# Optimization experiments

Measured on AMD Instinct MI355X. Metric: run time of the kernel, lower is better.

Reference implementation:

```python
import jax, jax.numpy as jnp
import numpy as np

B, T, D = 2, 2048, 1024
H, DH = 16, 64  # heads, head_dim; inner_dim = H*DH = D
EPS = 1e-6


def _rmsnorm(x, g):
    # torch.nn.RMSNorm over last dim with affine weight g
    return x * jax.lax.rsqrt(jnp.mean(x * x, axis=-1, keepdims=True) + EPS) * g


def _interleaved_rope(x, cos, sin):
    # x: [B, T, D]; pairs (x0, x1) rotated: rot = [-x1, x0, -x3, x2, ...]
    b, t, d = x.shape
    x2 = x.reshape(b, t, d // 2, 2)
    rot = jnp.stack([-x2[..., 1], x2[..., 0]], axis=-1).reshape(b, t, d)
    return x * cos + rot * sin


def setup_inputs() -> dict:
    key = jax.random.key(0)
    ks = jax.random.split(key, 8)
    hidden_states = jax.random.normal(ks[0], (B, T, D), dtype=jnp.float32)
    cos = jax.random.uniform(ks[1], (1, T, D), dtype=jnp.float32)
    sin = jax.random.uniform(ks[2], (1, T, D), dtype=jnp.float32)
    s = 0.02  # init scale for weights
    wq = jax.random.normal(ks[3], (D, D), dtype=jnp.float32) * s
    wk = jax.random.normal(ks[4], (D, D), dtype=jnp.float32) * s
    wv = jax.random.normal(ks[5], (D, D), dtype=jnp.float32) * s
    wo = jax.random.normal(ks[6], (D, D), dtype=jnp.float32) * s
    bq = jnp.zeros((D,), jnp.float32)
    bk = jnp.zeros((D,), jnp.float32)
    bv = jnp.zeros((D,), jnp.float32)
    bo = jnp.zeros((D,), jnp.float32)
    gq = jnp.ones((D,), jnp.float32)
    gk = jnp.ones((D,), jnp.float32)
    return {
        'hidden_states': hidden_states, 'cos': cos, 'sin': sin,
        'wq': wq, 'bq': bq, 'wk': wk, 'bk': bk, 'wv': wv, 'bv': bv,
        'gq': gq, 'gk': gk, 'wo': wo, 'bo': bo,
    }


def reference(hidden_states, cos, sin, wq, bq, wk, bk, wv, bv, gq, gk, wo, bo):
    # QKV projections (weights stored as [in, out]) + RMSNorm(q,k) + RoPE
    q = _interleaved_rope(_rmsnorm(hidden_states @ wq + bq, gq), cos, sin)
    k = _interleaved_rope(_rmsnorm(hidden_states @ wk + bk, gk), cos, sin)
    v = hidden_states @ wv + bv

    # split heads: [B, T, D] -> [B, H, T, DH]
    def split(x):
        return x.reshape(B, T, H, DH).transpose(0, 2, 1, 3)
    q, k, v = split(q), split(k), split(v)

    scale = 1.0 / jnp.sqrt(jnp.float32(DH))
    scores = jnp.einsum('bhqd,bhkd->bhqk', q, k) * scale
    attn = jax.nn.softmax(scores, axis=-1)
    out = jnp.einsum('bhqk,bhkd->bhqd', attn, v)

    # merge heads + output projection
    out = out.transpose(0, 2, 1, 3).reshape(B, T, D)
    return out @ wo + bo
```

## Files before the change

kernel.cpp:

```cpp
#include <hip/hip_runtime.h>

typedef _Float16 f16;
typedef _Float16 f16x8 __attribute__((ext_vector_type(8)));
typedef _Float16 f16x4 __attribute__((ext_vector_type(4)));
typedef _Float16 f16x2 __attribute__((ext_vector_type(2)));
typedef float f32x4 __attribute__((ext_vector_type(4)));

#define MFMA(a, b, c) __builtin_amdgcn_mfma_f32_16x16x32_f16(a, b, c, 0, 0, 0)
#define PKRTZ(a, b) __builtin_bit_cast(f16x2, __builtin_amdgcn_cvt_pkrtz(a, b))

__device__ __forceinline__ void gload16(const void* g, void* l) {
  __builtin_amdgcn_global_load_lds((const __attribute__((address_space(1))) char*)g,
                                   (__attribute__((address_space(3))) char*)l, 16, 0, 0);
}


__global__ __launch_bounds__(256) void k_cvt_hidden(const float* __restrict__ x, f16* __restrict__ y) {
  int i = blockIdx.x * 256 + threadIdx.x;
  float4 v = ((const float4*)x)[i];
  f16x4 h; h[0] = (f16)v.x; h[1] = (f16)v.y; h[2] = (f16)v.z; h[3] = (f16)v.w;
  ((f16x4*)y)[i] = h;
}

__global__ __launch_bounds__(256) void k_cvt_w(const float* __restrict__ w0, const float* __restrict__ w1,
                                               const float* __restrict__ w2, const float* __restrict__ w3,
                                               f16* __restrict__ wt) {
  int z = blockIdx.z;
  const float* w = z == 0 ? w0 : z == 1 ? w1 : z == 2 ? w2 : w3;
  f16* dst = wt + (size_t)z * 1024 * 1024;
  __shared__ float tile[64][65];
  int t = threadIdx.x;
  int k0 = blockIdx.x * 64, n0 = blockIdx.y * 64;
  int cr = t >> 4, cc = (t & 15) * 4;
#pragma unroll
  for (int p = 0; p < 4; p++) {
    int r = cr + p * 16;
    float4 v = *(const float4*)&w[(size_t)(k0 + r) * 1024 + n0 + cc];
    tile[r][cc + 0] = v.x; tile[r][cc + 1] = v.y; tile[r][cc + 2] = v.z; tile[r][cc + 3] = v.w;
  }
  __syncthreads();
#pragma unroll
  for (int p = 0; p < 4; p++) {
    int nn = cr + p * 16;
    f16x4 h;
    h[0] = (f16)tile[cc + 0][nn]; h[1] = (f16)tile[cc + 1][nn];
    h[2] = (f16)tile[cc + 2][nn]; h[3] = (f16)tile[cc + 3][nn];
    *(f16x4*)&dst[(size_t)(n0 + nn) * 1024 + k0 + cc] = h;
  }
}

template <bool OUTF32>
__device__ __forceinline__ void gemm_core(const f16* __restrict__ A, const f16* __restrict__ Wrows,
                                          const float* __restrict__ bias, int m0,
                                          f16* __restrict__ oh, float* __restrict__ of) {
  __shared__ f16 Al[2][128 * 64];
  __shared__ f16 Bl[2][128 * 64];
  const int t = threadIdx.x;
  const int lane = t & 63, wid = t >> 6;
  const int lr = lane & 15, lg = lane >> 4;
  const int wm = wid >> 1, wn = wid & 1;
  const int lrow = lane >> 3;
  const int cb = (((lane & 7) ^ lrow) << 4);

  f32x4 acc[4][4] = {};

  auto stage = [&](int k0, int bs) {
#pragma unroll
    for (int it = 0; it < 4; it++) {
      int rbase = it * 32 + wid * 8;
      int row = rbase + lrow;
      gload16((const char*)&A[(size_t)(m0 + row) * 1024 + k0] + cb, (char*)&Al[bs][0] + rbase * 128);
      gload16((const char*)&Wrows[(size_t)row * 1024 + k0] + cb, (char*)&Bl[bs][0] + rbase * 128);
    }
  };

  stage(0, 0);
  __syncthreads();
  int cur = 0;
  for (int k0 = 0; k0 < 1024; k0 += 64) {
    if (k0 + 64 < 1024) stage(k0 + 64, cur ^ 1);
    f16x8 af[2][4], bf[2][4];
#pragma unroll
    for (int x = 0; x < 4; x++) {
      int ra = wm * 64 + x * 16 + lr;
      int rb = wn * 64 + x * 16 + lr;
#pragma unroll
      for (int kh = 0; kh < 2; kh++) {
        int ca = (kh * 64 + lg * 16) ^ ((lr & 7) << 4);
        af[kh][x] = *(const f16x8*)((char*)&Al[cur][0] + ra * 128 + ca);
        bf[kh][x] = *(const f16x8*)((char*)&Bl[cur][0] + rb * 128 + ca);
      }
    }
    __builtin_amdgcn_s_setprio(1);
#pragma unroll
    for (int kh = 0; kh < 2; kh++)
#pragma unroll
      for (int mt = 0; mt < 4; mt++)
#pragma unroll
        for (int nt = 0; nt < 4; nt++)
          acc[mt][nt] = MFMA(af[kh][mt], bf[kh][nt], acc[mt][nt]);
    __builtin_amdgcn_s_setprio(0);
    __syncthreads();
    cur ^= 1;
  }
#pragma unroll
  for (int mt = 0; mt < 4; mt++) {
#pragma unroll
    for (int nt = 0; nt < 4; nt++) {
      int col = wn * 64 + nt * 16 + lr;
      float bcol = bias[col];
#pragma unroll
      for (int e = 0; e < 4; e++) {
        int row = m0 + wm * 64 + mt * 16 + lg * 4 + e;
        float val = acc[mt][nt][e] + bcol;
        if (OUTF32) of[(size_t)row * 1024 + col] = val;
        else        oh[(size_t)row * 1024 + col] = (f16)val;
      }
    }
  }
}

__global__ __launch_bounds__(256, 2) void k_gemm_qkv(const f16* __restrict__ A, const f16* __restrict__ wt,
                                                     const float* __restrict__ bq, const float* __restrict__ bk,
                                                     const float* __restrict__ bv,
                                                     f16* __restrict__ q, f16* __restrict__ k, f16* __restrict__ v) {
  int n0 = blockIdx.y * 128;
  int zsel = n0 >> 10, cbs = n0 & 1023;
  const float* bias = (zsel == 0 ? bq : zsel == 1 ? bk : bv) + cbs;
  f16* dst = (zsel == 0 ? q : zsel == 1 ? k : v) + cbs;
  gemm_core<false>(A, wt + (size_t)n0 * 1024, bias, blockIdx.x * 128, dst, nullptr);
}

__global__ __launch_bounds__(256, 2) void k_gemm_o(const f16* __restrict__ A, const f16* __restrict__ wt3,
                                                   const float* __restrict__ bo, float* __restrict__ out) {
  int n0 = blockIdx.y * 128;
  gemm_core<true>(A, wt3 + (size_t)n0 * 1024, bo + n0, blockIdx.x * 128, nullptr, out + n0);
}

__global__ __launch_bounds__(256) void k_normrope(f16* __restrict__ qh, f16* __restrict__ kh,
                                                  const float* __restrict__ gq, const float* __restrict__ gk,
                                                  const float* __restrict__ cs, const float* __restrict__ sn) {
  int row = blockIdx.x, which = blockIdx.y;
  f16* buf = which ? kh : qh;
  const float* g = which ? gk : gq;
  int t = threadIdx.x, c4 = t * 4;
  f16x4 xv = *(const f16x4*)&buf[(size_t)row * 1024 + c4];
  float x0 = xv[0], x1 = xv[1], x2 = xv[2], x3 = xv[3];
  float ss = x0 * x0 + x1 * x1 + x2 * x2 + x3 * x3;
#pragma unroll
  for (int off = 1; off < 64; off <<= 1) ss += __shfl_xor(ss, off);
  __shared__ float red[4];
  if ((t & 63) == 0) red[t >> 6] = ss;
  __syncthreads();
  float inv = rsqrtf((red[0] + red[1] + red[2] + red[3]) * (1.0f / 1024.0f) + 1e-6f);
  int tt = row & 2047;
  float4 cv = *(const float4*)&cs[(size_t)tt * 1024 + c4];
  float4 sv = *(const float4*)&sn[(size_t)tt * 1024 + c4];
  float4 gv = *(const float4*)&g[c4];
  float y0 = x0 * inv * gv.x, y1 = x1 * inv * gv.y, y2 = x2 * inv * gv.z, y3 = x3 * inv * gv.w;
  f16x4 ov;
  ov[0] = (f16)(y0 * cv.x - y1 * sv.x);
  ov[1] = (f16)(y1 * cv.y + y0 * sv.y);
  ov[2] = (f16)(y2 * cv.z - y3 * sv.z);
  ov[3] = (f16)(y3 * cv.w + y2 * sv.w);
  *(f16x4*)&buf[(size_t)row * 1024 + c4] = ov;
}

__global__ __launch_bounds__(256) void k_vtrans(const f16* __restrict__ vh, f16* __restrict__ vt) {
  __shared__ f16 tile[64][65];
  int t = threadIdx.x;
  int t0 = blockIdx.x * 64;
  int bh = blockIdx.y;
  int b = bh >> 4, h = bh & 15;
  int rr = t >> 3, c8 = (t & 7) * 8;
#pragma unroll
  for (int p = 0; p < 2; p++) {
    int r = p * 32 + rr;
    f16x8 v = *(const f16x8*)&vh[(size_t)(b * 2048 + t0 + r) * 1024 + h * 64 + c8];
#pragma unroll
    for (int j = 0; j < 8; j++) tile[r][c8 + j] = v[j];
  }
  __syncthreads();
#pragma unroll
  for (int p = 0; p < 2; p++) {
    int dh = p * 32 + rr;
    f16x8 o;
#pragma unroll
    for (int j = 0; j < 8; j++) o[j] = tile[c8 + j][dh];
    *(f16x8*)&vt[((size_t)bh * 64 + dh) * 2048 + t0 + c8] = o;
  }
}

#define ASWZ(row) ((((row) & 3) | (((row) & 8) >> 1)) << 4)

__global__ __launch_bounds__(256, 4) void k_attn(const f16* __restrict__ qh, const f16* __restrict__ kh,
                                                 const f16* __restrict__ vt,
                                                 f16* __restrict__ op0, f16* __restrict__ op1,
                                                 float* __restrict__ ml) {
  __shared__ f16 Kl[2][64 * 64];
  __shared__ f16 Vl[2][64 * 64];
  const int t = threadIdx.x;
  const int lane = t & 63, wid = t >> 6;
  const int lr = lane & 15, lg = lane >> 4;
  const int lgb = lg << 4;
  const int raw = blockIdx.x;
  const int mybh = ((raw & 7) << 2) | ((raw >> 3) & 3);
  const int half = (raw >> 5) & 1;
  const int myq = raw >> 6;
  const int b = mybh >> 4, h = mybh & 15;
  const int q0 = myq * 128 + wid * 32;
  const int kvbase = half << 10;
  f16* __restrict__ op = half ? op1 : op0;
  const f16* Qb = qh + ((size_t)(b * 2048 + q0)) * 1024 + h * 64;
  f16x8 qf[2][2];
#pragma unroll
  for (int g = 0; g < 2; g++) {
    qf[g][0] = *(const f16x8*)&Qb[(size_t)(g * 16 + lr) * 1024 + lg * 8];
    qf[g][1] = *(const f16x8*)&Qb[(size_t)(g * 16 + lr) * 1024 + 32 + lg * 8];
  }
  const f16* Kg = kh + ((size_t)b * 2048) * 1024 + h * 64;
  const f16* Vg = vt + ((size_t)mybh) * 64 * 2048;
  const int lrow = lane >> 3;
  const int sg = (lane & 7) << 4;
  const float sc = 0.125f * 1.44269504088896340736f;
  float m[2] = {-1e30f, -1e30f};
  f32x4 acc[2][4] = {};
  f32x4 accl[2] = {};
  const f16 ov1 = (lr == 0) ? (f16)1.0f : (f16)0.0f;
  const f16x8 onesf = {ov1, ov1, ov1, ov1, ov1, ov1, ov1, ov1};

  auto stage = [&](int kvo, int bs) {
#pragma unroll
    for (int i = 0; i < 2; i++) {
      int rbase = (i * 4 + wid) * 8;
      int row = rbase + lrow;
      int cswz = sg ^ ASWZ(row);
      gload16((const char*)(Kg + (size_t)(kvo + row) * 1024) + cswz, (char*)&Kl[bs][0] + rbase * 128);
      gload16((const char*)(Vg + (size_t)row * 2048 + kvo) + cswz, (char*)&Vl[bs][0] + rbase * 128);
    }
  };

  stage(kvbase, 0);
  __syncthreads();
  int cur = 0;

  for (int c = 0; c < 16; c++) {
    int kv0 = kvbase + c * 64;
    if (c + 1 < 16) stage(kv0 + 64, cur ^ 1);
    const char* Kb = (const char*)&Kl[cur][0];
    const char* Vb = (const char*)&Vl[cur][0];

    f32x4 s[2][4];
    __builtin_amdgcn_s_setprio(1);
#pragma unroll
    for (int ks = 0; ks < 4; ks++) {
      int key = ((lr >> 2) << 3) + (lr & 3) + ((ks & 1) << 2) + ((ks >> 1) << 5);
      int sw = ASWZ(key);
      f16x8 kf0 = *(const f16x8*)(Kb + key * 128 + (lgb ^ sw));
      f16x8 kf1 = *(const f16x8*)(Kb + key * 128 + ((64 + lgb) ^ sw));
#pragma unroll
      for (int g = 0; g < 2; g++) {
        f32x4 z = {};
        z = MFMA(kf0, qf[g][0], z);
        z = MFMA(kf1, qf[g][1], z);
        s[g][ks] = z;
      }
    }
    __builtin_amdgcn_s_setprio(0);

    union U { f16x8 v; f16x2 h[4]; } u[2][2];
#pragma unroll
    for (int g = 0; g < 2; g++) {
      float smax = fmaxf(fmaxf(s[g][0][0], s[g][0][1]), s[g][0][2]);
      smax = fmaxf(fmaxf(smax, s[g][0][3]), s[g][1][0]);
      smax = fmaxf(fmaxf(smax, s[g][1][1]), s[g][1][2]);
      smax = fmaxf(fmaxf(smax, s[g][1][3]), s[g][2][0]);
      smax = fmaxf(fmaxf(smax, s[g][2][1]), s[g][2][2]);
      smax = fmaxf(fmaxf(smax, s[g][2][3]), s[g][3][0]);
      smax = fmaxf(fmaxf(smax, s[g][3][1]), s[g][3][2]);
      smax = fmaxf(smax, s[g][3][3]);
      smax = fmaxf(smax, __shfl_xor(smax, 16));
      smax = fmaxf(smax, __shfl_xor(smax, 32));
      float smc = smax * sc;

      if (!__all(smc - m[g] <= 8.f)) {
        float mn = fmaxf(m[g], smc);
        float al = exp2f(m[g] - mn);
        m[g] = mn;
        float alq[4];
#pragma unroll
        for (int e = 0; e < 4; e++) alq[e] = __shfl(al, lg * 4 + e);
#pragma unroll
        for (int ds = 0; ds < 4; ds++)
#pragma unroll
          for (int e = 0; e < 4; e++) acc[g][ds][e] *= alq[e];
#pragma unroll
        for (int e = 0; e < 4; e++) accl[g][e] *= alq[e];
      }

#pragma unroll
      for (int ks = 0; ks < 4; ks++) {
        float p0 = exp2f(fmaf(s[g][ks][0], sc, -m[g]));
        float p1 = exp2f(fmaf(s[g][ks][1], sc, -m[g]));
        float p2 = exp2f(fmaf(s[g][ks][2], sc, -m[g]));
        float p3 = exp2f(fmaf(s[g][ks][3], sc, -m[g]));
        u[g][ks >> 1].h[(ks & 1) * 2 + 0] = PKRTZ(p0, p1);
        u[g][ks >> 1].h[(ks & 1) * 2 + 1] = PKRTZ(p2, p3);
      }
    }

    __builtin_amdgcn_s_setprio(1);
#pragma unroll
    for (int ds = 0; ds < 4; ds++) {
      int vrow = ds * 16 + lr;
      int sw = ASWZ(vrow);
      f16x8 vf0 = *(const f16x8*)(Vb + vrow * 128 + (lgb ^ sw));
      f16x8 vf1 = *(const f16x8*)(Vb + vrow * 128 + ((64 + lgb) ^ sw));
#pragma unroll
      for (int g = 0; g < 2; g++) {
        acc[g][ds] = MFMA(u[g][0].v, vf0, acc[g][ds]);
        acc[g][ds] = MFMA(u[g][1].v, vf1, acc[g][ds]);
      }
    }
#pragma unroll
    for (int g = 0; g < 2; g++) {
      accl[g] = MFMA(u[g][0].v, onesf, accl[g]);
      accl[g] = MFMA(u[g][1].v, onesf, accl[g]);
    }
    __builtin_amdgcn_s_setprio(0);

    __syncthreads();
    cur ^= 1;
  }

#pragma unroll
  for (int g = 0; g < 2; g++) {
    int qglob = mybh * 2048 + q0 + g * 16;
    if (lg == 0)
      ml[(size_t)((half << 16) + qglob + lr) * 2 + 0] = m[g];
    if (lr == 0) {
#pragma unroll
      for (int e = 0; e < 4; e++)
        ml[(size_t)((half << 16) + qglob + lg * 4 + e) * 2 + 1] = accl[g][e];
    }
#pragma unroll
    for (int e = 0; e < 4; e++) {
      float lf = 1.f / __shfl(accl[g][e], lg << 4);
      size_t row = (size_t)(b * 2048 + q0 + g * 16 + lg * 4 + e);
#pragma unroll
      for (int ds = 0; ds < 4; ds++)
        op[row * 1024 + h * 64 + ds * 16 + lr] = (f16)(acc[g][ds][e] * lf);
    }
  }
}

__global__ __launch_bounds__(256) void k_merge(const f16* __restrict__ op0, const f16* __restrict__ op1,
                                               const float* __restrict__ ml, f16* __restrict__ ao) {
  int i = blockIdx.x * 256 + threadIdx.x;
  int qid = i >> 3, seg = i & 7;
  float m0 = ml[(size_t)qid * 2], l0 = ml[(size_t)qid * 2 + 1];
  float m1 = ml[(size_t)(65536 + qid) * 2], l1 = ml[(size_t)(65536 + qid) * 2 + 1];
  float mm = fmaxf(m0, m1);
  float w0 = l0 * exp2f(m0 - mm), w1 = l1 * exp2f(m1 - mm);
  float inv = 1.f / (w0 + w1);
  w0 *= inv; w1 *= inv;
  int bh = qid >> 11, tt = qid & 2047;
  size_t addr = (((size_t)(bh >> 4) * 2048 + tt) * 1024 + (bh & 15) * 64 + seg * 8) / 8;
  f16x8 a = ((const f16x8*)op0)[addr];
  f16x8 bb = ((const f16x8*)op1)[addr];
  f16x8 o;
#pragma unroll
  for (int j = 0; j < 8; j++) o[j] = (f16)(w0 * (float)a[j] + w1 * (float)bb[j]);
  ((f16x8*)ao)[addr] = o;
}

extern "C" void kernel_launch(void* const* d_in, const int* in_sizes, int n_in,
                              void* d_out, int out_size, void* d_ws, size_t ws_size,
                              hipStream_t stream) {
  const float* hid  = (const float*)d_in[0];
  const float* cosb = (const float*)d_in[1];
  const float* sinb = (const float*)d_in[2];
  const float* wq = (const float*)d_in[3];
  const float* bq = (const float*)d_in[4];
  const float* wk = (const float*)d_in[5];
  const float* bk = (const float*)d_in[6];
  const float* wv = (const float*)d_in[7];
  const float* bv = (const float*)d_in[8];
  const float* gq = (const float*)d_in[9];
  const float* gk = (const float*)d_in[10];
  const float* wo = (const float*)d_in[11];
  const float* bo = (const float*)d_in[12];
  float* out = (float*)d_out;

  char* ws = (char*)d_ws;
  f16* aH  = (f16*)(ws);
  f16* wt  = (f16*)(ws + ((size_t)8 << 20));
  f16* qh  = (f16*)(ws + ((size_t)16 << 20));
  f16* khb = (f16*)(ws + ((size_t)24 << 20));
  f16* vhb = (f16*)(ws + ((size_t)32 << 20));
  f16* vtb = (f16*)(ws + ((size_t)40 << 20));
  f16* ao  = (f16*)(ws + ((size_t)48 << 20));
  float* ml = (float*)(ws + ((size_t)56 << 20));

  k_cvt_hidden<<<dim3(4096), dim3(256), 0, stream>>>(hid, aH);
  k_cvt_w<<<dim3(16, 16, 4), dim3(256), 0, stream>>>(wq, wk, wv, wo, wt);
  k_gemm_qkv<<<dim3(32, 24), dim3(256), 0, stream>>>(aH, wt, bq, bk, bv, qh, khb, vhb);
  k_normrope<<<dim3(4096, 2), dim3(256), 0, stream>>>(qh, khb, gq, gk, cosb, sinb);
  k_vtrans<<<dim3(32, 32), dim3(256), 0, stream>>>(vhb, vtb);
  k_attn<<<dim3(1024), dim3(256), 0, stream>>>(qh, khb, vtb, vhb, aH, ml);
  k_merge<<<dim3(2048), dim3(256), 0, stream>>>(vhb, aH, ml, ao);
  k_gemm_o<<<dim3(32, 8), dim3(256), 0, stream>>>(ao, wt + (size_t)3 * 1024 * 1024, bo, out);
}
```

Baseline: 145.1 us.

## Fuse split-KV merge into output GEMM and merge small prep kernels

The two-half attention merge now happens inside the output projection GEMM. It loads both partial outputs and their (m, l) statistics into registers, combines them, and writes the A tile to LDS while the B tile streams in asynchronously. This removes the separate merge kernel and the round trip of its intermediate buffer. The hidden/weight conversion kernels and the norm-rope/V-transpose kernels are also combined into single launches, cutting launch count. In exchange, the A operand of the output GEMM no longer uses async global-to-LDS loads. Extra register-held loads and exp math may lengthen the GEMM loop, and the merge is recomputed by each of the 8 column blocks.

```diff
diff --git a/kernel.cpp b/kernel.cpp
--- a/kernel.cpp
+++ b/kernel.cpp
@@ -15,21 +15,26 @@
 }
 
 
-__global__ __launch_bounds__(256) void k_cvt_hidden(const float* __restrict__ x, f16* __restrict__ y) {
-  int i = blockIdx.x * 256 + threadIdx.x;
-  float4 v = ((const float4*)x)[i];
-  f16x4 h; h[0] = (f16)v.x; h[1] = (f16)v.y; h[2] = (f16)v.z; h[3] = (f16)v.w;
-  ((f16x4*)y)[i] = h;
-}
-
-__global__ __launch_bounds__(256) void k_cvt_w(const float* __restrict__ w0, const float* __restrict__ w1,
-                                               const float* __restrict__ w2, const float* __restrict__ w3,
-                                               f16* __restrict__ wt) {
+__global__ __launch_bounds__(256) void k_prep(const float* __restrict__ hid,
+                                              const float* __restrict__ w0, const float* __restrict__ w1,
+                                              const float* __restrict__ w2, const float* __restrict__ w3,
+                                              f16* __restrict__ aH, f16* __restrict__ wt) {
   int z = blockIdx.z;
+  int t = threadIdx.x;
+  if (z == 4) {
+    int base = (blockIdx.y * 16 + blockIdx.x) * 256 + t;
+#pragma unroll
+    for (int j = 0; j < 16; j++) {
+      int i = base + j * 65536;
+      float4 v = ((const float4*)hid)[i];
+      f16x4 h; h[0] = (f16)v.x; h[1] = (f16)v.y; h[2] = (f16)v.z; h[3] = (f16)v.w;
+      ((f16x4*)aH)[i] = h;
+    }
+    return;
+  }
   const float* w = z == 0 ? w0 : z == 1 ? w1 : z == 2 ? w2 : w3;
   f16* dst = wt + (size_t)z * 1024 * 1024;
   __shared__ float tile[64][65];
-  int t = threadIdx.x;
   int k0 = blockIdx.x * 64, n0 = blockIdx.y * 64;
   int cr = t >> 4, cc = (t & 15) * 4;
 #pragma unroll
@@ -49,10 +54,9 @@
   }
 }
 
-template <bool OUTF32>
 __device__ __forceinline__ void gemm_core(const f16* __restrict__ A, const f16* __restrict__ Wrows,
                                           const float* __restrict__ bias, int m0,
-                                          f16* __restrict__ oh, float* __restrict__ of) {
+                                          f16* __restrict__ oh) {
   __shared__ f16 Al[2][128 * 64];
   __shared__ f16 Bl[2][128 * 64];
   const int t = threadIdx.x;
@@ -112,9 +116,7 @@
 #pragma unroll
       for (int e = 0; e < 4; e++) {
         int row = m0 + wm * 64 + mt * 16 + lg * 4 + e;
-        float val = acc[mt][nt][e] + bcol;
-        if (OUTF32) of[(size_t)row * 1024 + col] = val;
-        else        oh[(size_t)row * 1024 + col] = (f16)val;
+        oh[(size_t)row * 1024 + col] = (f16)(acc[mt][nt][e] + bcol);
       }
     }
   }
@@ -128,28 +130,155 @@
   int zsel = n0 >> 10, cbs = n0 & 1023;
   const float* bias = (zsel == 0 ? bq : zsel == 1 ? bk : bv) + cbs;
   f16* dst = (zsel == 0 ? q : zsel == 1 ? k : v) + cbs;
-  gemm_core<false>(A, wt + (size_t)n0 * 1024, bias, blockIdx.x * 128, dst, nullptr);
-}
-
-__global__ __launch_bounds__(256, 2) void k_gemm_o(const f16* __restrict__ A, const f16* __restrict__ wt3,
+  gemm_core(A, wt + (size_t)n0 * 1024, bias, blockIdx.x * 128, dst);
+}
+
+__global__ __launch_bounds__(256, 2) void k_gemm_o(const f16* __restrict__ op0, const f16* __restrict__ op1,
+                                                   const float* __restrict__ ml,
+                                                   const f16* __restrict__ wt3,
                                                    const float* __restrict__ bo, float* __restrict__ out) {
-  int n0 = blockIdx.y * 128;
-  gemm_core<true>(A, wt3 + (size_t)n0 * 1024, bo + n0, blockIdx.x * 128, nullptr, out + n0);
-}
-
-__global__ __launch_bounds__(256) void k_normrope(f16* __restrict__ qh, f16* __restrict__ kh,
-                                                  const float* __restrict__ gq, const float* __restrict__ gk,
-                                                  const float* __restrict__ cs, const float* __restrict__ sn) {
-  int row = blockIdx.x, which = blockIdx.y;
+  __shared__ f16 Al[2][128 * 64];
+  __shared__ f16 Bl[2][128 * 64];
+  const int t = threadIdx.x;
+  const int lane = t & 63, wid = t >> 6;
+  const int lr = lane & 15, lg = lane >> 4;
+  const int wm = wid >> 1, wn = wid & 1;
+  const int lrow = lane >> 3;
+  const int cb = (((lane & 7) ^ lrow) << 4);
+  const int m0 = blockIdx.x * 128, n0 = blockIdx.y * 128;
+  const f16* Wrows = wt3 + (size_t)n0 * 1024;
+  const float* bias = bo + n0;
+  float* of = out + n0;
+
+  f32x4 acc[4][4] = {};
+  f16x8 a0r[4], a1r[4];
+  float2 ml0r[4], ml1r[4];
+
+  auto stageB = [&](int k0, int bs) {
+#pragma unroll
+    for (int it = 0; it < 4; it++) {
+      int rbase = it * 32 + wid * 8;
+      gload16((const char*)&Wrows[(size_t)(rbase + lrow) * 1024 + k0] + cb, (char*)&Bl[bs][0] + rbase * 128);
+    }
+  };
+  auto loadA = [&](int k0) {
+    int head = k0 >> 6;
+#pragma unroll
+    for (int it = 0; it < 4; it++) {
+      int rg = m0 + it * 32 + wid * 8 + lrow;
+      size_t off = (size_t)rg * 1024 + k0 + (cb >> 1);
+      a0r[it] = *(const f16x8*)&op0[off];
+      a1r[it] = *(const f16x8*)&op1[off];
+      int qid = (((rg >> 11) << 4) + head) * 2048 + (rg & 2047);
+      ml0r[it] = *(const float2*)&ml[(size_t)qid * 2];
+      ml1r[it] = *(const float2*)&ml[(size_t)(65536 + qid) * 2];
+    }
+  };
+  auto writeA = [&](int bs) {
+#pragma unroll
+    for (int it = 0; it < 4; it++) {
+      float mm = fmaxf(ml0r[it].x, ml1r[it].x);
+      float w0 = ml0r[it].y * exp2f(ml0r[it].x - mm);
+      float w1 = ml1r[it].y * exp2f(ml1r[it].x - mm);
+      float inv = 1.f / (w0 + w1);
+      w0 *= inv; w1 *= inv;
+      f16x8 o;
+#pragma unroll
+      for (int j = 0; j < 8; j++)
+        o[j] = (f16)(w0 * (float)a0r[it][j] + w1 * (float)a1r[it][j]);
+      int rbase = it * 32 + wid * 8;
+      *(f16x8*)((char*)&Al[bs][0] + (rbase + lrow) * 128 + (lane & 7) * 16) = o;
+    }
+  };
+
+  loadA(0); stageB(0, 0); writeA(0);
+  __syncthreads();
+  int cur = 0;
+  for (int k0 = 0; k0 < 1024; k0 += 64) {
+    bool pre = (k0 + 64 < 1024);
+    if (pre) { loadA(k0 + 64); stageB(k0 + 64, cur ^ 1); }
+    f16x8 af[2][4], bf[2][4];
+#pragma unroll
+    for (int x = 0; x < 4; x++) {
+      int ra = wm * 64 + x * 16 + lr;
+      int rb = wn * 64 + x * 16 + lr;
+#pragma unroll
+      for (int kh = 0; kh < 2; kh++) {
+        int ca = (kh * 64 + lg * 16) ^ ((lr & 7) << 4);
+        af[kh][x] = *(const f16x8*)((char*)&Al[cur][0] + ra * 128 + ca);
+        bf[kh][x] = *(const f16x8*)((char*)&Bl[cur][0] + rb * 128 + ca);
+      }
+    }
+    __builtin_amdgcn_s_setprio(1);
+#pragma unroll
+    for (int kh = 0; kh < 2; kh++)
+#pragma unroll
+      for (int mt = 0; mt < 4; mt++)
+#pragma unroll
+        for (int nt = 0; nt < 4; nt++)
+          acc[mt][nt] = MFMA(af[kh][mt], bf[kh][nt], acc[mt][nt]);
+    __builtin_amdgcn_s_setprio(0);
+    if (pre) writeA(cur ^ 1);
+    __syncthreads();
+    cur ^= 1;
+  }
+#pragma unroll
+  for (int mt = 0; mt < 4; mt++) {
+#pragma unroll
+    for (int nt = 0; nt < 4; nt++) {
+      int col = wn * 64 + nt * 16 + lr;
+      float bcol = bias[col];
+#pragma unroll
+      for (int e = 0; e < 4; e++) {
+        int row = m0 + wm * 64 + mt * 16 + lg * 4 + e;
+        of[(size_t)row * 1024 + col] = acc[mt][nt][e] + bcol;
+      }
+    }
+  }
+}
+
+__global__ __launch_bounds__(256) void k_nrv(f16* __restrict__ qh, f16* __restrict__ kh,
+                                             const float* __restrict__ gq, const float* __restrict__ gk,
+                                             const float* __restrict__ cs, const float* __restrict__ sn,
+                                             const f16* __restrict__ vh, f16* __restrict__ vt) {
+  __shared__ float redtile[64][65];
+  int which = blockIdx.y;
+  int t = threadIdx.x;
+  if (which == 2) {
+    if (blockIdx.x >= 1024) return;
+    f16* tile = (f16*)&redtile[0][0];
+    int bh = blockIdx.x & 31;
+    int t0 = (blockIdx.x >> 5) * 64;
+    int b = bh >> 4, h = bh & 15;
+    int rr = t >> 3, c8 = (t & 7) * 8;
+#pragma unroll
+    for (int p = 0; p < 2; p++) {
+      int r = p * 32 + rr;
+      f16x8 v = *(const f16x8*)&vh[(size_t)(b * 2048 + t0 + r) * 1024 + h * 64 + c8];
+#pragma unroll
+      for (int j = 0; j < 8; j++) tile[r * 66 + c8 + j] = v[j];
+    }
+    __syncthreads();
+#pragma unroll
+    for (int p = 0; p < 2; p++) {
+      int dh = p * 32 + rr;
+      f16x8 o;
+#pragma unroll
+      for (int j = 0; j < 8; j++) o[j] = tile[(c8 + j) * 66 + dh];
+      *(f16x8*)&vt[((size_t)bh * 64 + dh) * 2048 + t0 + c8] = o;
+    }
+    return;
+  }
+  int row = blockIdx.x;
   f16* buf = which ? kh : qh;
   const float* g = which ? gk : gq;
-  int t = threadIdx.x, c4 = t * 4;
+  int c4 = t * 4;
   f16x4 xv = *(const f16x4*)&buf[(size_t)row * 1024 + c4];
   float x0 = xv[0], x1 = xv[1], x2 = xv[2], x3 = xv[3];
   float ss = x0 * x0 + x1 * x1 + x2 * x2 + x3 * x3;
 #pragma unroll
   for (int off = 1; off < 64; off <<= 1) ss += __shfl_xor(ss, off);
-  __shared__ float red[4];
+  float* red = &redtile[0][0];
   if ((t & 63) == 0) red[t >> 6] = ss;
   __syncthreads();
   float inv = rsqrtf((red[0] + red[1] + red[2] + red[3]) * (1.0f / 1024.0f) + 1e-6f);
@@ -164,31 +293,6 @@
   ov[2] = (f16)(y2 * cv.z - y3 * sv.z);
   ov[3] = (f16)(y3 * cv.w + y2 * sv.w);
   *(f16x4*)&buf[(size_t)row * 1024 + c4] = ov;
-}
-
-__global__ __launch_bounds__(256) void k_vtrans(const f16* __restrict__ vh, f16* __restrict__ vt) {
-  __shared__ f16 tile[64][65];
-  int t = threadIdx.x;
-  int t0 = blockIdx.x * 64;
-  int bh = blockIdx.y;
-  int b = bh >> 4, h = bh & 15;
-  int rr = t >> 3, c8 = (t & 7) * 8;
-#pragma unroll
-  for (int p = 0; p < 2; p++) {
-    int r = p * 32 + rr;
-    f16x8 v = *(const f16x8*)&vh[(size_t)(b * 2048 + t0 + r) * 1024 + h * 64 + c8];
-#pragma unroll
-    for (int j = 0; j < 8; j++) tile[r][c8 + j] = v[j];
-  }
-  __syncthreads();
-#pragma unroll
-  for (int p = 0; p < 2; p++) {
-    int dh = p * 32 + rr;
-    f16x8 o;
-#pragma unroll
-    for (int j = 0; j < 8; j++) o[j] = tile[c8 + j][dh];
-    *(f16x8*)&vt[((size_t)bh * 64 + dh) * 2048 + t0 + c8] = o;
-  }
 }
 
 #define ASWZ(row) ((((row) & 3) | (((row) & 8) >> 1)) << 4)
@@ -354,26 +458,6 @@
   }
 }
 
-__global__ __launch_bounds__(256) void k_merge(const f16* __restrict__ op0, const f16* __restrict__ op1,
-                                               const float* __restrict__ ml, f16* __restrict__ ao) {
-  int i = blockIdx.x * 256 + threadIdx.x;
-  int qid = i >> 3, seg = i & 7;
-  float m0 = ml[(size_t)qid * 2], l0 = ml[(size_t)qid * 2 + 1];
-  float m1 = ml[(size_t)(65536 + qid) * 2], l1 = ml[(size_t)(65536 + qid) * 2 + 1];
-  float mm = fmaxf(m0, m1);
-  float w0 = l0 * exp2f(m0 - mm), w1 = l1 * exp2f(m1 - mm);
-  float inv = 1.f / (w0 + w1);
-  w0 *= inv; w1 *= inv;
-  int bh = qid >> 11, tt = qid & 2047;
-  size_t addr = (((size_t)(bh >> 4) * 2048 + tt) * 1024 + (bh & 15) * 64 + seg * 8) / 8;
-  f16x8 a = ((const f16x8*)op0)[addr];
-  f16x8 bb = ((const f16x8*)op1)[addr];
-  f16x8 o;
-#pragma unroll
-  for (int j = 0; j < 8; j++) o[j] = (f16)(w0 * (float)a[j] + w1 * (float)bb[j]);
-  ((f16x8*)ao)[addr] = o;
-}
-
 extern "C" void kernel_launch(void* const* d_in, const int* in_sizes, int n_in,
                               void* d_out, int out_size, void* d_ws, size_t ws_size,
                               hipStream_t stream) {
@@ -399,15 +483,11 @@
   f16* khb = (f16*)(ws + ((size_t)24 << 20));
   f16* vhb = (f16*)(ws + ((size_t)32 << 20));
   f16* vtb = (f16*)(ws + ((size_t)40 << 20));
-  f16* ao  = (f16*)(ws + ((size_t)48 << 20));
-  float* ml = (float*)(ws + ((size_t)56 << 20));
-
-  k_cvt_hidden<<<dim3(4096), dim3(256), 0, stream>>>(hid, aH);
-  k_cvt_w<<<dim3(16, 16, 4), dim3(256), 0, stream>>>(wq, wk, wv, wo, wt);
+  float* ml = (float*)(ws + ((size_t)48 << 20));
+
+  k_prep<<<dim3(16, 16, 5), dim3(256), 0, stream>>>(hid, wq, wk, wv, wo, aH, wt);
   k_gemm_qkv<<<dim3(32, 24), dim3(256), 0, stream>>>(aH, wt, bq, bk, bv, qh, khb, vhb);
-  k_normrope<<<dim3(4096, 2), dim3(256), 0, stream>>>(qh, khb, gq, gk, cosb, sinb);
-  k_vtrans<<<dim3(32, 32), dim3(256), 0, stream>>>(vhb, vtb);
+  k_nrv<<<dim3(4096, 3), dim3(256), 0, stream>>>(qh, khb, gq, gk, cosb, sinb, vhb, vtb);
   k_attn<<<dim3(1024), dim3(256), 0, stream>>>(qh, khb, vtb, vhb, aH, ml);
-  k_merge<<<dim3(2048), dim3(256), 0, stream>>>(vhb, aH, ml, ao);
-  k_gemm_o<<<dim3(32, 8), dim3(256), 0, stream>>>(ao, wt + (size_t)3 * 1024 * 1024, bo, out);
-}
+  k_gemm_o<<<dim3(32, 8), dim3(256), 0, stream>>>(vhb, aH, ml, wt + (size_t)3 * 1024 * 1024, bo, out);
+}
```

Measured after the change: 155.1 us. 6.9% more time.
